# Kernel optimization log

Hardware: AMD Instinct MI355X
Metric: run time of the kernel (lower is better)

## Reference

```python
import jax, jax.numpy as jnp
import numpy as np

N_NODES = 50000
N_EDGES = 800000
D_MODEL = 128
N_HEADS = 4
N_LAYERS = 2
F_HEAD = D_MODEL // N_HEADS


def setup_inputs() -> dict:
    key = jax.random.key(0)
    ks = jax.random.split(key, 6)
    x = jax.random.normal(ks[0], (N_NODES, D_MODEL), dtype=jnp.float32)
    edge_index = jax.random.randint(ks[1], (2, N_EDGES), 0, N_NODES, dtype=jnp.int64)
    scale = 1.0 / np.sqrt(D_MODEL)
    W = jax.random.normal(ks[2], (N_LAYERS, D_MODEL, D_MODEL), dtype=jnp.float32) * scale
    a_src = jax.random.normal(ks[3], (N_LAYERS, N_HEADS, F_HEAD), dtype=jnp.float32) * scale
    a_dst = jax.random.normal(ks[4], (N_LAYERS, N_HEADS, F_HEAD), dtype=jnp.float32) * scale
    b = jnp.zeros((N_LAYERS, D_MODEL), dtype=jnp.float32)
    return {"x": x, "edge_index": edge_index, "W": W, "a_src": a_src, "a_dst": a_dst, "b": b}


def _gat_layer(x, src, dst, W_l, a_src_l, a_dst_l, b_l, apply_act):
    N = x.shape[0]
    H, F = a_src_l.shape
    # projected node features, split into heads: [N, H, F]
    h = (x @ W_l).reshape(N, H, F)
    # per-node attention contributions: [N, H]
    alpha_s = jnp.einsum("nhf,hf->nh", h, a_src_l)
    alpha_d = jnp.einsum("nhf,hf->nh", h, a_dst_l)
    # per-edge raw scores, LeakyReLU(0.2): [E, H]
    e = jax.nn.leaky_relu(alpha_s[src] + alpha_d[dst], negative_slope=0.2)
    # numerically-stable segment softmax over edges grouped by target node
    e_max = jax.ops.segment_max(e, dst, num_segments=N)
    e_exp = jnp.exp(e - e_max[dst])
    denom = jax.ops.segment_sum(e_exp, dst, num_segments=N)
    alpha = e_exp / (denom[dst] + 1e-16)  # [E, H]
    # gather source features, weight, scatter-add to targets
    msg = h[src] * alpha[:, :, None]  # [E, H, F]
    out = jax.ops.segment_sum(msg, dst, num_segments=N).reshape(N, H * F)
    out = out + x + b_l  # skip connection (dims match) + bias
    return jax.nn.elu(out) if apply_act else out


def reference(x, edge_index, W, a_src, a_dst, b):
    src, dst = edge_index[0], edge_index[1]
    L = W.shape[0]
    for l in range(L):
        x = _gat_layer(x, src, dst, W[l], a_src[l], a_dst[l], b[l], apply_act=(l < L - 1))
    return x
```

## Files before the change

kernel.cpp:

```cpp
#include <hip/hip_runtime.h>
#include <math.h>

constexpr int NN = 50000;
constexpr int NE = 800000;
constexpr int D  = 128;
constexpr int NH = 4;
constexpr int NBUK = (NN + 255) / 256;
constexpr int EPB  = 2048;
constexpr int NPB  = (NE + EPB - 1) / EPB;
constexpr int CAPS = 4608;
constexpr int FR_PER_LAYER = 9 * 4 * 64;
constexpr int RBLK = (2 * FR_PER_LAYER) / 256;

typedef __attribute__((ext_vector_type(8))) short short8v;
typedef __attribute__((ext_vector_type(4))) float f32x4;

__device__ inline unsigned short rne_bf16(float f) {
    unsigned bits = __float_as_uint(f);
    return (unsigned short)((bits + 0x7FFFu + ((bits >> 16) & 1u)) >> 16);
}

#define DOT2BF(accv, pa, pb) \
    asm("v_dot2_f32_bf16 %0, %1, %2, %0" : "+v"(accv) : "v"(pa), "v"(pb))

__device__ __forceinline__ void repack_body(
    int tid, const float* __restrict__ W, const float* __restrict__ a_src,
    const float* __restrict__ a_dst, unsigned short* __restrict__ Wpk)
{
    int layer = tid / FR_PER_LAYER;
    int rest  = tid % FR_PER_LAYER;
    int tile  = rest >> 8;
    int kstep = (rest >> 6) & 3;
    int lane  = rest & 63;
    int col   = lane & 15;
    int kbase = kstep * 32 + (lane >> 4) * 8;
    const float* Wl = W + (size_t)layer * D * D;
    unsigned short v[8];
    if (tile < 8) {
        int c = tile * 16 + col;
        #pragma unroll
        for (int j = 0; j < 8; ++j) v[j] = rne_bf16(Wl[(kbase + j) * D + c]);
    } else {
        #pragma unroll
        for (int j = 0; j < 8; ++j) v[j] = 0;
        if (col < 8) {
            const float* av = ((col < 4) ? a_src : a_dst) + layer * D + (col & 3) * 32;
            const int hbase = (col & 3) * 32;
            for (int j = 0; j < 8; ++j) {
                float sum = 0.f;
                const float* wr = Wl + (size_t)(kbase + j) * D + hbase;
                #pragma unroll
                for (int jj = 0; jj < 32; ++jj) sum = fmaf(wr[jj], av[jj], sum);
                v[j] = rne_bf16(sum);
            }
        }
    }
    *(uint4*)(Wpk + (size_t)tid * 8) = *(const uint4*)v;
}

__global__ __launch_bounds__(256) void prep_kernel(
    const float* __restrict__ W, const float* __restrict__ a_src,
    const float* __restrict__ a_dst, unsigned short* __restrict__ Wpk,
    const int* __restrict__ src, const int* __restrict__ dst,
    unsigned* __restrict__ outbuf, int* __restrict__ cnts,
    int* __restrict__ lofs)
{
    __shared__ union {
        struct { unsigned stage[EPB]; int cnt[NBUK]; int fill[NBUK]; int sc[256]; } p;
        int dummy;
    } sm;
    if (blockIdx.x < RBLK) {
        repack_body(blockIdx.x * 256 + threadIdx.x, W, a_src, a_dst, Wpk);
        return;
    }
    const int pb = blockIdx.x - RBLK;
    const int t  = threadIdx.x;
    for (int i = t; i < NBUK; i += 256) sm.p.cnt[i] = 0;
    __syncthreads();
    const int base = pb * EPB;
    const int tot  = min(NE - base, EPB);
    unsigned pk[8]; int bk[8];
    #pragma unroll
    for (int i = 0; i < 8; ++i) {
        int e = base + i * 256 + t;
        bool ok = (e < NE);
        int s = ok ? src[e] : 0;
        int d = ok ? dst[e] : 0;
        bk[i] = d >> 8;
        pk[i] = (unsigned)s | ((unsigned)(d & 255) << 16) | ((unsigned)bk[i] << 24);
        if (ok) atomicAdd(&sm.p.cnt[bk[i]], 1);
    }
    __syncthreads();
    int v = (t < NBUK) ? sm.p.cnt[t] : 0;
    sm.p.sc[t] = v;
    __syncthreads();
    for (int off = 1; off < 256; off <<= 1) {
        int u = (t >= off) ? sm.p.sc[t - off] : 0;
        __syncthreads();
        sm.p.sc[t] += u;
        __syncthreads();
    }
    const int excl = sm.p.sc[t] - v;
    if (t < NBUK) {
        sm.p.fill[t] = excl;
        cnts[t * NPB + pb] = v;
        lofs[t * NPB + pb] = excl;
    }
    __syncthreads();
    #pragma unroll
    for (int i = 0; i < 8; ++i) {
        int e = base + i * 256 + t;
        if (e < NE) {
            int pos = atomicAdd(&sm.p.fill[bk[i]], 1);
            sm.p.stage[pos] = pk[i];
        }
    }
    __syncthreads();
    for (int i = t; i < tot; i += 256) outbuf[base + i] = sm.p.stage[i];
}

template<int BF16IN>
__device__ __forceinline__ void gemm_body(
    int blk, unsigned short* __restrict__ xl, const void* __restrict__ xin,
    const unsigned short* __restrict__ Wpk, unsigned short* __restrict__ hb,
    float* __restrict__ alpha_s, float* __restrict__ alpha_d)
{
    const int t = threadIdx.x;
    const int row0 = blk * 64;

    if constexpr (BF16IN) {
        const unsigned short* xb = (const unsigned short*)xin;
        #pragma unroll
        for (int it = 0; it < 4; ++it) {
            int idx = it * 256 + t;
            int r   = idx >> 4;
            int c8  = (idx & 15) * 8;
            int n   = row0 + r;
            uint4 v = {0u, 0u, 0u, 0u};
            if (n < NN) v = *(const uint4*)(xb + (size_t)n * D + c8);
            *(uint4*)(xl + r * 128 + (c8 ^ ((r & 7) << 3))) = v;
        }
    } else {
        const float* xf = (const float*)xin;
        #pragma unroll
        for (int it = 0; it < 8; ++it) {
            int idx = it * 256 + t;
            int r   = idx >> 5;
            int c4  = (idx & 31) * 4;
            int n   = row0 + r;
            float4 v;
            if (n < NN) v = *(const float4*)(xf + (size_t)n * D + c4);
            else { v.x = 0.f; v.y = 0.f; v.z = 0.f; v.w = 0.f; }
            unsigned p0 = ((unsigned)rne_bf16(v.y) << 16) | rne_bf16(v.x);
            unsigned p1 = ((unsigned)rne_bf16(v.w) << 16) | rne_bf16(v.z);
            uint2 pv; pv.x = p0; pv.y = p1;
            *(uint2*)(xl + r * 128 + (c4 ^ ((r & 7) << 3))) = pv;
        }
    }
    __syncthreads();

    const int wv  = t >> 6;
    const int l   = t & 63;
    const int l15 = l & 15;
    const int g   = l >> 4;
    const int strip = wv * 16;
    const int arow  = strip + l15;

    f32x4 acc[9];
    #pragma unroll
    for (int i = 0; i < 9; ++i) acc[i] = (f32x4){0.f, 0.f, 0.f, 0.f};

    #pragma unroll
    for (int ks = 0; ks < 4; ++ks) {
        const int k0 = ks * 32 + g * 8;
        short8v a = *(const short8v*)(xl + arow * 128 + (k0 ^ ((arow & 7) << 3)));
        #pragma unroll
        for (int tl = 0; tl < 9; ++tl) {
            short8v b = *(const short8v*)(Wpk + ((size_t)(tl * 4 + ks) * 64 + l) * 8);
            acc[tl] = __builtin_amdgcn_mfma_f32_16x16x32_bf16(a, b, acc[tl], 0, 0, 0);
        }
    }

    #pragma unroll
    for (int r = 0; r < 4; ++r) {
        const int n = row0 + strip + g * 4 + r;
        if (n < NN) {
            #pragma unroll
            for (int tl = 0; tl < 8; ++tl)
                hb[(size_t)n * D + tl * 16 + l15] = rne_bf16(acc[tl][r]);
            const float av = acc[8][r];
            if (l15 < 4)      alpha_s[n * NH + l15]       = av;
            else if (l15 < 8) alpha_d[n * NH + (l15 - 4)] = av;
        }
    }
}

template<int BF16IN>
__global__ __launch_bounds__(256) void sort_gemm_kernel(
    const unsigned* __restrict__ outbuf, const int* __restrict__ cnts,
    const int* __restrict__ lofs, int2* __restrict__ rowse,
    unsigned short* __restrict__ srcs, const void* __restrict__ xin,
    const unsigned short* __restrict__ Wpk, unsigned short* __restrict__ hb,
    float* __restrict__ alpha_s, float* __restrict__ alpha_d)
{
    __shared__ union {
        struct { unsigned stage[CAPS]; int hist[256]; int run[256]; int sc[256]; int cursor; } s;
        unsigned short xl[64 * 128];
    } sm;

    if (blockIdx.x >= NBUK) {
        gemm_body<BF16IN>(blockIdx.x - NBUK, sm.xl, xin, Wpk, hb, alpha_s, alpha_d);
        return;
    }
    const int b = blockIdx.x;
    const int t = threadIdx.x;
    if (t == 0) sm.s.cursor = 0;
    sm.s.hist[t] = 0;
    __syncthreads();
    for (int pb = t; pb < NPB; pb += 256) {
        int len = cnts[b * NPB + pb];
        if (len > 0) {
            int off = lofs[b * NPB + pb];
            int pos = atomicAdd(&sm.s.cursor, len);
            const unsigned* sp = outbuf + pb * EPB + off;
            for (int k = 0; k < len; ++k)
                if (pos + k < CAPS) sm.s.stage[pos + k] = sp[k];
        }
    }
    __syncthreads();
    const int tot = min(sm.s.cursor, CAPS);
    for (int i = t; i < tot; i += 256)
        atomicAdd(&sm.s.hist[(sm.s.stage[i] >> 16) & 255], 1);
    __syncthreads();
    int v = sm.s.hist[t];
    sm.s.sc[t] = v;
    __syncthreads();
    for (int off = 1; off < 256; off <<= 1) {
        int u = (t >= off) ? sm.s.sc[t - off] : 0;
        __syncthreads();
        sm.s.sc[t] += u;
        __syncthreads();
    }
    const int excl = sm.s.sc[t] - v;
    const int node = b * 256 + t;
    if (node < NN) {
        int2 se; se.x = b * CAPS + excl; se.y = b * CAPS + excl + v;
        rowse[node] = se;
    }
    sm.s.run[t] = excl;
    __syncthreads();
    for (int i = t; i < tot; i += 256) {
        unsigned p = sm.s.stage[i];
        int pos = atomicAdd(&sm.s.run[(p >> 16) & 255], 1);
        srcs[b * CAPS + pos] = (unsigned short)(p & 0xFFFFu);
    }
}

template<int BF16IN>
__global__ __launch_bounds__(256) void gemm_alpha_kernel(
    const void* __restrict__ xin, const unsigned short* __restrict__ Wpk,
    unsigned short* __restrict__ hb, float* __restrict__ alpha_s,
    float* __restrict__ alpha_d)
{
    __shared__ unsigned short xl[64 * 128];
    gemm_body<BF16IN>(blockIdx.x, xl, xin, Wpk, hb, alpha_s, alpha_d);
}

#define SHUF2(MI, SA, SB, WP) {                                          \
    int eA = lb + (MI), eB = eA + 1;                                     \
    SA = __shfl(msrc, eA); SB = __shfl(msrc, eB);                        \
    unsigned a01 = (unsigned)__shfl((int)uw01, eA);                      \
    unsigned a23 = (unsigned)__shfl((int)uw23, eA);                      \
    unsigned c01 = (unsigned)__shfl((int)uw01, eB);                      \
    unsigned c23 = (unsigned)__shfl((int)uw23, eB);                      \
    unsigned uwA = (head < 2) ? a01 : a23;                               \
    unsigned uwB = (head < 2) ? c01 : c23;                               \
    WP = __builtin_amdgcn_perm(uwB, uwA, wsel); }

#define ROWLD(S) (*(const uint4*)(hb + ((size_t)(S) << 7) + (ql << 3)))

#define DOT2BLOCK(WP, HA, HB) {                                               \
    DOT2BF(den, WP, ones);                                                    \
    unsigned p_;                                                              \
    p_ = __builtin_amdgcn_perm(HB.x, HA.x, 0x05040100u); DOT2BF(acc[0], p_, WP); \
    p_ = __builtin_amdgcn_perm(HB.x, HA.x, 0x07060302u); DOT2BF(acc[1], p_, WP); \
    p_ = __builtin_amdgcn_perm(HB.y, HA.y, 0x05040100u); DOT2BF(acc[2], p_, WP); \
    p_ = __builtin_amdgcn_perm(HB.y, HA.y, 0x07060302u); DOT2BF(acc[3], p_, WP); \
    p_ = __builtin_amdgcn_perm(HB.z, HA.z, 0x05040100u); DOT2BF(acc[4], p_, WP); \
    p_ = __builtin_amdgcn_perm(HB.z, HA.z, 0x07060302u); DOT2BF(acc[5], p_, WP); \
    p_ = __builtin_amdgcn_perm(HB.w, HA.w, 0x05040100u); DOT2BF(acc[6], p_, WP); \
    p_ = __builtin_amdgcn_perm(HB.w, HA.w, 0x07060302u); DOT2BF(acc[7], p_, WP); }

template<int IN_BF16, int OUT_BF16, int ACT>
__global__ __launch_bounds__(256) void gather_kernel(
    const unsigned short* __restrict__ hb, const float* __restrict__ alpha_s,
    const float* __restrict__ alpha_d, const int2* __restrict__ rowse,
    const unsigned short* __restrict__ srcs, const void* __restrict__ x_in,
    const float* __restrict__ bias, void* __restrict__ out)
{
    const int lane = threadIdx.x & 63;
    const int q    = lane >> 4;
    const int ql   = lane & 15;
    const int head = ql >> 2;
    const int lb   = q * 16;
    const int n = blockIdx.x * 16 + (threadIdx.x >> 6) * 4 + q;
    if (n >= NN) return;

    const int2 se = rowse[n];
    const int start = se.x, end = se.y;
    const float4 ad4 = *(const float4*)&alpha_d[n * NH];
    const unsigned wsel = (head & 1) ? 0x07060302u : 0x05040100u;
    const unsigned ones = 0x3F803F80u;

    float acc[8];
    #pragma unroll
    for (int c = 0; c < 8; ++c) acc[c] = 0.f;
    float den = 0.f;

    for (int base = start; base < end; base += 16) {
        const int cnt = min(16, end - base);
        int msrc = 0;
        unsigned uw01 = 0, uw23 = 0;
        if (ql < cnt) {
            msrc = srcs[base + ql];
            const float4 as4 = *(const float4*)&alpha_s[msrc * NH];
            float e0 = as4.x + ad4.x; e0 = (e0 > 0.f) ? e0 : 0.2f * e0;
            float e1 = as4.y + ad4.y; e1 = (e1 > 0.f) ? e1 : 0.2f * e1;
            float e2 = as4.z + ad4.z; e2 = (e2 > 0.f) ? e2 : 0.2f * e2;
            float e3 = as4.w + ad4.w; e3 = (e3 > 0.f) ? e3 : 0.2f * e3;
            float w0 = __expf(e0), w1 = __expf(e1);
            float w2 = __expf(e2), w3 = __expf(e3);
            uw01 = ((unsigned)rne_bf16(w1) << 16) | rne_bf16(w0);
            uw23 = ((unsigned)rne_bf16(w3) << 16) | rne_bf16(w2);
        }
        const int mm = (cnt + 1) & ~1;

        int sxa, sxb, sya, syb;
        unsigned wpX, wpY;
        uint4 hxa, hxb, hya, hyb;
        SHUF2(0, sxa, sxb, wpX);
        hxa = ROWLD(sxa); hxb = ROWLD(sxb);
        if (mm > 2) {
            SHUF2(2, sya, syb, wpY);
            hya = ROWLD(sya); hyb = ROWLD(syb);
        }
        int m = 0;
        while (true) {
            DOT2BLOCK(wpX, hxa, hxb);
            m += 2;
            if (m >= mm) break;
            if (m + 2 < mm) {
                SHUF2(m + 2, sxa, sxb, wpX);
                hxa = ROWLD(sxa); hxb = ROWLD(sxb);
            }
            DOT2BLOCK(wpY, hya, hyb);
            m += 2;
            if (m >= mm) break;
            if (m + 2 < mm) {
                SHUF2(m + 2, sya, syb, wpY);
                hya = ROWLD(sya); hyb = ROWLD(syb);
            }
        }
    }

    const float inv = 1.f / (den + 1e-16f);
    const size_t o8 = (size_t)n * D + ql * 8;
    float xi[8];
    if constexpr (IN_BF16) {
        const uint4 xv = *(const uint4*)((const unsigned short*)x_in + o8);
        xi[0] = __uint_as_float(xv.x << 16);
        xi[1] = __uint_as_float(xv.x & 0xFFFF0000u);
        xi[2] = __uint_as_float(xv.y << 16);
        xi[3] = __uint_as_float(xv.y & 0xFFFF0000u);
        xi[4] = __uint_as_float(xv.z << 16);
        xi[5] = __uint_as_float(xv.z & 0xFFFF0000u);
        xi[6] = __uint_as_float(xv.w << 16);
        xi[7] = __uint_as_float(xv.w & 0xFFFF0000u);
    } else {
        const float4 a = *(const float4*)((const float*)x_in + o8);
        const float4 b = *(const float4*)((const float*)x_in + o8 + 4);
        xi[0]=a.x; xi[1]=a.y; xi[2]=a.z; xi[3]=a.w;
        xi[4]=b.x; xi[5]=b.y; xi[6]=b.z; xi[7]=b.w;
    }
    const float4 ba = *(const float4*)(bias + ql * 8);
    const float4 bb = *(const float4*)(bias + ql * 8 + 4);
    const float bi[8] = {ba.x, ba.y, ba.z, ba.w, bb.x, bb.y, bb.z, bb.w};
    float o[8];
    #pragma unroll
    for (int c = 0; c < 8; ++c) {
        float v = fmaf(acc[c], inv, xi[c]) + bi[c];
        if constexpr (ACT) v = (v > 0.f) ? v : (__expf(v) - 1.f);
        o[c] = v;
    }
    if constexpr (OUT_BF16) {
        unsigned short ov[8];
        #pragma unroll
        for (int c = 0; c < 8; ++c) ov[c] = rne_bf16(o[c]);
        *(uint4*)((unsigned short*)out + o8) = *(const uint4*)ov;
    } else {
        float4 oa = {o[0], o[1], o[2], o[3]};
        float4 ob = {o[4], o[5], o[6], o[7]};
        *(float4*)((float*)out + o8)     = oa;
        *(float4*)((float*)out + o8 + 4) = ob;
    }
}

extern "C" void kernel_launch(void* const* d_in, const int* in_sizes, int n_in,
                              void* d_out, int out_size, void* d_ws, size_t ws_size,
                              hipStream_t stream) {
    const float* x     = (const float*)d_in[0];
    const int*   ei    = (const int*)d_in[1];
    const float* W     = (const float*)d_in[2];
    const float* a_src = (const float*)d_in[3];
    const float* a_dst = (const float*)d_in[4];
    const float* bias  = (const float*)d_in[5];
    float* outp = (float*)d_out;

    const int* e_src = ei;
    const int* e_dst = ei + NE;

    char* base = (char*)d_ws;
    unsigned short* hb  = (unsigned short*)(base);
    unsigned short* x1b = (unsigned short*)(base + 12800000);
    float* al_s      = (float*)(base + 25600000);
    float* al_d      = (float*)(base + 26400000);
    int2*  rowse     = (int2*) (base + 27200000);
    unsigned short* srcs = (unsigned short*)(base + 27600000);
    unsigned* outbuf = (unsigned*)(base + 29406336);
    int* cnts        = (int*)  (base + 32609408);
    int* lofs        = (int*)  (base + 32915952);
    unsigned short* Wpk = (unsigned short*)(base + 33222496);

    prep_kernel<<<RBLK + NPB, 256, 0, stream>>>(W, a_src, a_dst, Wpk,
                                                e_src, e_dst, outbuf, cnts, lofs);

    const int gemm_blocks   = (NN + 63) / 64;
    const int gather_blocks = (NN + 15) / 16;

    sort_gemm_kernel<0><<<NBUK + gemm_blocks, 256, 0, stream>>>(
        outbuf, cnts, lofs, rowse, srcs, x, Wpk, hb, al_s, al_d);

    gather_kernel<0, 1, 1><<<gather_blocks, 256, 0, stream>>>(
        hb, al_s, al_d, rowse, srcs, x, bias, x1b);

    gemm_alpha_kernel<1><<<gemm_blocks, 256, 0, stream>>>(
        x1b, Wpk + (size_t)FR_PER_LAYER * 8, hb, al_s, al_d);

    gather_kernel<1, 0, 0><<<gather_blocks, 256, 0, stream>>>(
        hb, al_s, al_d, rowse, srcs, x1b, bias + D, outp);
}
```

Baseline: 125.0 us.

## Partition each node's edge list by source half to localize gather reads

The bucket sort now keys on destination node plus whether the source index is in the lower or upper half of the node range, and records a midpoint per node. The gather kernel processes the two halves separately, so at any moment all waves tend to read h rows from one half of the feature table. The aim is better L2/MALL locality for the random row gathers. The cost is an extra midp array and split loops that may add partial 16-edge batches per node.

```diff
diff --git a/kernel.cpp b/kernel.cpp
--- a/kernel.cpp
+++ b/kernel.cpp
@@ -9,6 +9,7 @@
 constexpr int EPB  = 2048;
 constexpr int NPB  = (NE + EPB - 1) / EPB;
 constexpr int CAPS = 4608;
+constexpr int SRC_MID = 25000;
 constexpr int FR_PER_LAYER = 9 * 4 * 64;
 constexpr int RBLK = (2 * FR_PER_LAYER) / 256;
 
@@ -199,12 +200,13 @@
 __global__ __launch_bounds__(256) void sort_gemm_kernel(
     const unsigned* __restrict__ outbuf, const int* __restrict__ cnts,
     const int* __restrict__ lofs, int2* __restrict__ rowse,
-    unsigned short* __restrict__ srcs, const void* __restrict__ xin,
-    const unsigned short* __restrict__ Wpk, unsigned short* __restrict__ hb,
-    float* __restrict__ alpha_s, float* __restrict__ alpha_d)
+    int* __restrict__ midp, unsigned short* __restrict__ srcs,
+    const void* __restrict__ xin, const unsigned short* __restrict__ Wpk,
+    unsigned short* __restrict__ hb, float* __restrict__ alpha_s,
+    float* __restrict__ alpha_d)
 {
     __shared__ union {
-        struct { unsigned stage[CAPS]; int hist[256]; int run[256]; int sc[256]; int cursor; } s;
+        struct { unsigned stage[CAPS]; int hist[512]; int run[512]; int sc[256]; int cursor; } s;
         unsigned short xl[64 * 128];
     } sm;
 
@@ -215,7 +217,7 @@
     const int b = blockIdx.x;
     const int t = threadIdx.x;
     if (t == 0) sm.s.cursor = 0;
-    sm.s.hist[t] = 0;
+    sm.s.hist[t] = 0; sm.s.hist[t + 256] = 0;
     __syncthreads();
     for (int pb = t; pb < NPB; pb += 256) {
         int len = cnts[b * NPB + pb];
@@ -229,11 +231,16 @@
     }
     __syncthreads();
     const int tot = min(sm.s.cursor, CAPS);
-    for (int i = t; i < tot; i += 256)
-        atomicAdd(&sm.s.hist[(sm.s.stage[i] >> 16) & 255], 1);
-    __syncthreads();
-    int v = sm.s.hist[t];
-    sm.s.sc[t] = v;
+    for (int i = t; i < tot; i += 256) {
+        unsigned p = sm.s.stage[i];
+        int key = ((int)((p >> 16) & 255u) << 1) | (int)((p & 0xFFFFu) >= (unsigned)SRC_MID);
+        atomicAdd(&sm.s.hist[key], 1);
+    }
+    __syncthreads();
+    const int v0 = sm.s.hist[2 * t];
+    const int v1 = sm.s.hist[2 * t + 1];
+    const int pv = v0 + v1;
+    sm.s.sc[t] = pv;
     __syncthreads();
     for (int off = 1; off < 256; off <<= 1) {
         int u = (t >= off) ? sm.s.sc[t - off] : 0;
@@ -241,17 +248,20 @@
         sm.s.sc[t] += u;
         __syncthreads();
     }
-    const int excl = sm.s.sc[t] - v;
+    const int pexcl = sm.s.sc[t] - pv;
     const int node = b * 256 + t;
     if (node < NN) {
-        int2 se; se.x = b * CAPS + excl; se.y = b * CAPS + excl + v;
+        int2 se; se.x = b * CAPS + pexcl; se.y = b * CAPS + pexcl + pv;
         rowse[node] = se;
-    }
-    sm.s.run[t] = excl;
+        midp[node]  = se.x + v0;
+    }
+    sm.s.run[2 * t]     = pexcl;
+    sm.s.run[2 * t + 1] = pexcl + v0;
     __syncthreads();
     for (int i = t; i < tot; i += 256) {
         unsigned p = sm.s.stage[i];
-        int pos = atomicAdd(&sm.s.run[(p >> 16) & 255], 1);
+        int key = ((int)((p >> 16) & 255u) << 1) | (int)((p & 0xFFFFu) >= (unsigned)SRC_MID);
+        int pos = atomicAdd(&sm.s.run[key], 1);
         srcs[b * CAPS + pos] = (unsigned short)(p & 0xFFFFu);
     }
 }
@@ -295,8 +305,9 @@
 __global__ __launch_bounds__(256) void gather_kernel(
     const unsigned short* __restrict__ hb, const float* __restrict__ alpha_s,
     const float* __restrict__ alpha_d, const int2* __restrict__ rowse,
-    const unsigned short* __restrict__ srcs, const void* __restrict__ x_in,
-    const float* __restrict__ bias, void* __restrict__ out)
+    const int* __restrict__ midp, const unsigned short* __restrict__ srcs,
+    const void* __restrict__ x_in, const float* __restrict__ bias,
+    void* __restrict__ out)
 {
     const int lane = threadIdx.x & 63;
     const int q    = lane >> 4;
@@ -307,7 +318,7 @@
     if (n >= NN) return;
 
     const int2 se = rowse[n];
-    const int start = se.x, end = se.y;
+    const int md  = midp[n];
     const float4 ad4 = *(const float4*)&alpha_d[n * NH];
     const unsigned wsel = (head & 1) ? 0x07060302u : 0x05040100u;
     const unsigned ones = 0x3F803F80u;
@@ -317,51 +328,55 @@
     for (int c = 0; c < 8; ++c) acc[c] = 0.f;
     float den = 0.f;
 
-    for (int base = start; base < end; base += 16) {
-        const int cnt = min(16, end - base);
-        int msrc = 0;
-        unsigned uw01 = 0, uw23 = 0;
-        if (ql < cnt) {
-            msrc = srcs[base + ql];
-            const float4 as4 = *(const float4*)&alpha_s[msrc * NH];
-            float e0 = as4.x + ad4.x; e0 = (e0 > 0.f) ? e0 : 0.2f * e0;
-            float e1 = as4.y + ad4.y; e1 = (e1 > 0.f) ? e1 : 0.2f * e1;
-            float e2 = as4.z + ad4.z; e2 = (e2 > 0.f) ? e2 : 0.2f * e2;
-            float e3 = as4.w + ad4.w; e3 = (e3 > 0.f) ? e3 : 0.2f * e3;
-            float w0 = __expf(e0), w1 = __expf(e1);
-            float w2 = __expf(e2), w3 = __expf(e3);
-            uw01 = ((unsigned)rne_bf16(w1) << 16) | rne_bf16(w0);
-            uw23 = ((unsigned)rne_bf16(w3) << 16) | rne_bf16(w2);
-        }
-        const int mm = (cnt + 1) & ~1;
-
-        int sxa, sxb, sya, syb;
-        unsigned wpX, wpY;
-        uint4 hxa, hxb, hya, hyb;
-        SHUF2(0, sxa, sxb, wpX);
-        hxa = ROWLD(sxa); hxb = ROWLD(sxb);
-        if (mm > 2) {
-            SHUF2(2, sya, syb, wpY);
-            hya = ROWLD(sya); hyb = ROWLD(syb);
-        }
-        int m = 0;
-        while (true) {
-            DOT2BLOCK(wpX, hxa, hxb);
-            m += 2;
-            if (m >= mm) break;
-            if (m + 2 < mm) {
-                SHUF2(m + 2, sxa, sxb, wpX);
-                hxa = ROWLD(sxa); hxb = ROWLD(sxb);
+    auto run_range = [&](int rs, int re) {
+        for (int base = rs; base < re; base += 16) {
+            const int cnt = min(16, re - base);
+            int msrc = 0;
+            unsigned uw01 = 0, uw23 = 0;
+            if (ql < cnt) {
+                msrc = srcs[base + ql];
+                const float4 as4 = *(const float4*)&alpha_s[msrc * NH];
+                float e0 = as4.x + ad4.x; e0 = (e0 > 0.f) ? e0 : 0.2f * e0;
+                float e1 = as4.y + ad4.y; e1 = (e1 > 0.f) ? e1 : 0.2f * e1;
+                float e2 = as4.z + ad4.z; e2 = (e2 > 0.f) ? e2 : 0.2f * e2;
+                float e3 = as4.w + ad4.w; e3 = (e3 > 0.f) ? e3 : 0.2f * e3;
+                float w0 = __expf(e0), w1 = __expf(e1);
+                float w2 = __expf(e2), w3 = __expf(e3);
+                uw01 = ((unsigned)rne_bf16(w1) << 16) | rne_bf16(w0);
+                uw23 = ((unsigned)rne_bf16(w3) << 16) | rne_bf16(w2);
             }
-            DOT2BLOCK(wpY, hya, hyb);
-            m += 2;
-            if (m >= mm) break;
-            if (m + 2 < mm) {
-                SHUF2(m + 2, sya, syb, wpY);
+            const int mm = (cnt + 1) & ~1;
+
+            int sxa, sxb, sya, syb;
+            unsigned wpX, wpY;
+            uint4 hxa, hxb, hya, hyb;
+            SHUF2(0, sxa, sxb, wpX);
+            hxa = ROWLD(sxa); hxb = ROWLD(sxb);
+            if (mm > 2) {
+                SHUF2(2, sya, syb, wpY);
                 hya = ROWLD(sya); hyb = ROWLD(syb);
             }
-        }
-    }
+            int m = 0;
+            while (true) {
+                DOT2BLOCK(wpX, hxa, hxb);
+                m += 2;
+                if (m >= mm) break;
+                if (m + 2 < mm) {
+                    SHUF2(m + 2, sxa, sxb, wpX);
+                    hxa = ROWLD(sxa); hxb = ROWLD(sxb);
+                }
+                DOT2BLOCK(wpY, hya, hyb);
+                m += 2;
+                if (m >= mm) break;
+                if (m + 2 < mm) {
+                    SHUF2(m + 2, sya, syb, wpY);
+                    hya = ROWLD(sya); hyb = ROWLD(syb);
+                }
+            }
+        }
+    };
+    run_range(se.x, md);
+    run_range(md, se.y);
 
     const float inv = 1.f / (den + 1e-16f);
     const size_t o8 = (size_t)n * D + ql * 8;
@@ -425,11 +440,12 @@
     float* al_s      = (float*)(base + 25600000);
     float* al_d      = (float*)(base + 26400000);
     int2*  rowse     = (int2*) (base + 27200000);
-    unsigned short* srcs = (unsigned short*)(base + 27600000);
-    unsigned* outbuf = (unsigned*)(base + 29406336);
-    int* cnts        = (int*)  (base + 32609408);
-    int* lofs        = (int*)  (base + 32915952);
-    unsigned short* Wpk = (unsigned short*)(base + 33222496);
+    int*   midp      = (int*)  (base + 27600064);
+    unsigned short* srcs = (unsigned short*)(base + 27800064);
+    unsigned* outbuf = (unsigned*)(base + 29606400);
+    int* cnts        = (int*)  (base + 32809472);
+    int* lofs        = (int*)  (base + 33116016);
+    unsigned short* Wpk = (unsigned short*)(base + 33422560);
 
     prep_kernel<<<RBLK + NPB, 256, 0, stream>>>(W, a_src, a_dst, Wpk,
                                                 e_src, e_dst, outbuf, cnts, lofs);
@@ -438,14 +454,14 @@
     const int gather_blocks = (NN + 15) / 16;
 
     sort_gemm_kernel<0><<<NBUK + gemm_blocks, 256, 0, stream>>>(
-        outbuf, cnts, lofs, rowse, srcs, x, Wpk, hb, al_s, al_d);
+        outbuf, cnts, lofs, rowse, midp, srcs, x, Wpk, hb, al_s, al_d);
 
     gather_kernel<0, 1, 1><<<gather_blocks, 256, 0, stream>>>(
-        hb, al_s, al_d, rowse, srcs, x, bias, x1b);
+        hb, al_s, al_d, rowse, midp, srcs, x, bias, x1b);
 
     gemm_alpha_kernel<1><<<gemm_blocks, 256, 0, stream>>>(
         x1b, Wpk + (size_t)FR_PER_LAYER * 8, hb, al_s, al_d);
 
     gather_kernel<1, 0, 0><<<gather_blocks, 256, 0, stream>>>(
-        hb, al_s, al_d, rowse, srcs, x1b, bias + D, outp);
-}
+        hb, al_s, al_d, rowse, midp, srcs, x1b, bias + D, outp);
+}
```

After: 129.2 us. +3.3%, slower.
